# Kernel optimization log

Measured on AMD Instinct MI355X. Metric: run time of the kernel, lower is better.

The kernel has to match this reference:

```python
import jax, jax.numpy as jnp
import numpy as np

ALPHA, GAMMA = 0.25, 2.0
SPARSITY_PENALTY = 1.0
FOCAL_W, SPARSITY_W, CONC_W = 1.0, 0.8, 1.5
CONC_INNER_W = 1.0  # ConcentrationLoss(concentration_weight=1.0)


def setup_inputs() -> dict:
    key = jax.random.key(0)
    k1, k2 = jax.random.split(key)
    B, C, H, W = 16, 20, 256, 256
    pred = jax.random.normal(k1, (B, C, H, W), dtype=jnp.float32)
    target = (jax.random.uniform(k2, (B, C, H, W)) < 0.05).astype(jnp.float32)
    return {"pred": pred, "target": target}


def reference(pred, target):
    B, C, H, W = pred.shape
    p = jax.nn.sigmoid(pred)

    # ---- Focal loss ----
    is_pos = target == 1.0
    pt = jnp.where(is_pos, p, 1.0 - p)
    alpha_t = jnp.where(is_pos, ALPHA, 1.0 - ALPHA)
    focal = jnp.mean(-alpha_t * (1.0 - pt) ** GAMMA * jnp.log(pt + 1e-8))

    # ---- Sparsity loss ----
    sparsity = jnp.mean((pred - target) ** 2) + SPARSITY_PENALTY * jnp.mean(jnp.abs(pred))

    # ---- Concentration loss (vectorized over (b, c)) ----
    y = jnp.arange(H, dtype=jnp.float32)[:, None]   # [H,1]
    x = jnp.arange(W, dtype=jnp.float32)[None, :]   # [1,W]
    mass = target.sum(axis=(2, 3))                  # [B,C]
    valid = mass > 0
    safe_mass = jnp.where(valid, mass, 1.0)
    cy = jnp.einsum('bchw,hw->bc', target, jnp.broadcast_to(y, (H, W))) / safe_mass
    cx = jnp.einsum('bchw,hw->bc', target, jnp.broadcast_to(x, (H, W))) / safe_mass
    # squared distance to per-(b,c) target centroid: [B,C,H,W]
    dsq = (y[None, None] - cy[:, :, None, None]) ** 2 + (x[None, None] - cx[:, :, None, None]) ** 2
    per_sample = jnp.mean(p * dsq, axis=(2, 3))     # [B,C]
    n_valid = valid.sum()
    conc_sum = jnp.sum(jnp.where(valid, per_sample, 0.0))
    concentration = jnp.where(
        n_valid > 0,
        conc_sum / jnp.maximum(n_valid, 1).astype(jnp.float32),
        0.0,
    ) * CONC_INNER_W

    total = FOCAL_W * focal + SPARSITY_W * sparsity + CONC_W * concentration
    return total, focal, sparsity, concentration
```

## Files before the change

kernel.cpp:

```cpp
#include <hip/hip_runtime.h>
#include <math.h>

constexpr int Bn = 16, Cn = 20, Hn = 256, Wn = 256;
constexpr int BCn = Bn * Cn;
constexpr int HWn = Hn * Wn;
constexpr int SPLIT = 8;
constexpr int NBLK = BCn * SPLIT;
constexpr int CHUNK = HWn / SPLIT;
constexpr int TPB = 256;
constexpr int V4 = CHUNK / (TPB * 4);
constexpr int NSLOT = 10;

__device__ inline float wave_reduce(float v) {
    #pragma unroll
    for (int o = 32; o > 0; o >>= 1) v += __shfl_down(v, o, 64);
    return v;
}

__global__ __launch_bounds__(TPB) void partials_kernel(
        const float* __restrict__ pred, const float* __restrict__ target,
        float* __restrict__ ws) {
    const int blk = blockIdx.x;
    const int bc = blk >> 3;
    const int chunk = blk & (SPLIT - 1);
    const long long base = (long long)bc * HWn + (long long)chunk * CHUNK;
    const float4* __restrict__ p4 = (const float4*)(pred + base);
    const float4* __restrict__ t4 = (const float4*)(target + base);
    const int tid = threadIdx.x;

    float acc[NSLOT];
    #pragma unroll
    for (int k = 0; k < NSLOT; k++) acc[k] = 0.f;

    const int e_base = chunk * CHUNK + tid * 4;
    const float x0 = (float)(e_base & 255);
    const float x1 = x0 + 1.f, x2 = x0 + 2.f, x3 = x0 + 3.f;
    const float xs[4]  = {x0, x1, x2, x3};
    const float xxs[4] = {x0 * x0, x1 * x1, x2 * x2, x3 * x3};
    float y = (float)(e_base >> 8);

    float4 pc = p4[tid];
    float4 tc = t4[tid];

    #pragma unroll
    for (int i = 0; i < V4; i++) {
        float4 pn, tn;
        if (i + 1 < V4) {
            pn = p4[(i + 1) * TPB + tid];
            tn = t4[(i + 1) * TPB + tid];
        }
        const float yy = y * y;
        const float pvals[4] = {pc.x, pc.y, pc.z, pc.w};
        const float tvals[4] = {tc.x, tc.y, tc.z, tc.w};
        #pragma unroll
        for (int j = 0; j < 4; j++) {
            const float v = pvals[j];
            const float t = tvals[j];
            const float x = xs[j];
            const float e = __expf(-v);
            const float p = __builtin_amdgcn_rcpf(1.0f + e);
            const bool pos = (t > 0.5f);
            const float lp = __logf(p);
            const float lpt = pos ? lp : lp - v;
            const float om = pos ? 1.0f - p : p;
            const float at = pos ? 0.25f : 0.75f;
            acc[7] = fmaf(at * lpt, om * om, acc[7]);
            const float d = v - t;
            acc[8] = fmaf(d, d, acc[8]);
            acc[9] += fabsf(v);
            acc[0] += t;
            acc[1] = fmaf(t, y, acc[1]);
            acc[2] = fmaf(t, x, acc[2]);
            acc[3] += p;
            acc[4] = fmaf(p, y, acc[4]);
            acc[5] = fmaf(p, x, acc[5]);
            acc[6] = fmaf(p, yy + xxs[j], acc[6]);
        }
        y += 4.0f;
        if (i + 1 < V4) { pc = pn; tc = tn; }
    }

    __shared__ float lds[TPB / 64][NSLOT];
    const int lane = tid & 63, wave = tid >> 6;
    #pragma unroll
    for (int k = 0; k < NSLOT; k++) {
        const float r = wave_reduce(acc[k]);
        if (lane == 0) lds[wave][k] = r;
    }
    __syncthreads();
    if (tid < NSLOT) {
        float s = 0.f;
        #pragma unroll
        for (int w = 0; w < TPB / 64; w++) s += lds[w][tid];
        ws[blk * NSLOT + tid] = s;
    }
}

__global__ __launch_bounds__(512) void finalize_kernel(
        const float* __restrict__ ws, float* __restrict__ out) {
    const int tid = threadIdx.x;

    float conc_sum = 0.f, nvalid = 0.f;
    if (tid < BCn) {
        float mass = 0, sty = 0, stx = 0, sp = 0, spy = 0, spx = 0, sprr = 0;
        for (int s = 0; s < SPLIT; s++) {
            const float* w = ws + (size_t)(tid * SPLIT + s) * NSLOT;
            mass += w[0]; sty += w[1]; stx += w[2]; sp += w[3];
            spy  += w[4]; spx += w[5]; sprr += w[6];
        }
        const bool valid = mass > 0.f;
        const float sm = valid ? mass : 1.0f;
        const float cy = sty / sm, cx = stx / sm;
        const float pdsq = sprr - 2.f * cy * spy - 2.f * cx * spx
                         + (cy * cy + cx * cx) * sp;
        conc_sum = valid ? (pdsq / (float)HWn) : 0.f;
        nvalid   = valid ? 1.f : 0.f;
    }

    float foc = 0.f, sq = 0.f, ab = 0.f;
    for (int blk = tid; blk < NBLK; blk += 512) {
        const float* w = ws + (size_t)blk * NSLOT;
        foc += w[7]; sq += w[8]; ab += w[9];
    }

    __shared__ float lds[8][5];
    const int lane = tid & 63, wave = tid >> 6;
    float vals[5] = {conc_sum, nvalid, foc, sq, ab};
    #pragma unroll
    for (int k = 0; k < 5; k++) {
        const float r = wave_reduce(vals[k]);
        if (lane == 0) lds[wave][k] = r;
    }
    __syncthreads();

    if (tid == 0) {
        float tot[5];
        #pragma unroll
        for (int k = 0; k < 5; k++) {
            float s = 0.f;
            #pragma unroll
            for (int w = 0; w < 8; w++) s += lds[w][k];
            tot[k] = s;
        }
        const float NTOT = (float)Bn * Cn * Hn * Wn;
        const float focal = -tot[2] / NTOT;
        const float sparsity = tot[3] / NTOT + tot[4] / NTOT;
        const float concentration =
            (tot[1] > 0.f) ? (tot[0] / fmaxf(tot[1], 1.f)) : 0.f;
        const float total = 1.0f * focal + 0.8f * sparsity + 1.5f * concentration;
        out[0] = total;
        out[1] = focal;
        out[2] = sparsity;
        out[3] = concentration;
    }
}

extern "C" void kernel_launch(void* const* d_in, const int* in_sizes, int n_in,
                              void* d_out, int out_size, void* d_ws, size_t ws_size,
                              hipStream_t stream) {
    const float* pred   = (const float*)d_in[0];
    const float* target = (const float*)d_in[1];
    float* out = (float*)d_out;
    float* ws  = (float*)d_ws;

    partials_kernel<<<NBLK, TPB, 0, stream>>>(pred, target, ws);
    finalize_kernel<<<1, 512, 0, stream>>>(ws, out);
}
```

Before: 187.9 us.

## Use branchless log2-domain focal math, halve split, transpose workspace layout

Rewrites the per-element focal loss in base-2 (exp2/log2 builtins) with branchless fmaf selects driven by the binary target, and applies the ln2 scale once in the finalize step. Row-constant y terms are hoisted out of the inner 4-element loop by accumulating per-float4 sums of t and p. SPLIT drops from 8 to 4, so each block handles twice as many elements, and launch bounds now request 8 blocks per CU. The workspace is stored slot-major so the 320-thread finalize reads it with coalesced float4 loads. The branchless math relies on targets being exactly 0 or 1, and fewer blocks means less latency hiding.

```diff
diff --git a/kernel.cpp b/kernel.cpp
--- a/kernel.cpp
+++ b/kernel.cpp
@@ -4,7 +4,7 @@
 constexpr int Bn = 16, Cn = 20, Hn = 256, Wn = 256;
 constexpr int BCn = Bn * Cn;
 constexpr int HWn = Hn * Wn;
-constexpr int SPLIT = 8;
+constexpr int SPLIT = 4;
 constexpr int NBLK = BCn * SPLIT;
 constexpr int CHUNK = HWn / SPLIT;
 constexpr int TPB = 256;
@@ -17,11 +17,11 @@
     return v;
 }
 
-__global__ __launch_bounds__(TPB) void partials_kernel(
+__global__ __launch_bounds__(TPB, 8) void partials_kernel(
         const float* __restrict__ pred, const float* __restrict__ target,
         float* __restrict__ ws) {
     const int blk = blockIdx.x;
-    const int bc = blk >> 3;
+    const int bc = blk >> 2;
     const int chunk = blk & (SPLIT - 1);
     const long long base = (long long)bc * HWn + (long long)chunk * CHUNK;
     const float4* __restrict__ p4 = (const float4*)(pred + base);
@@ -34,10 +34,11 @@
 
     const int e_base = chunk * CHUNK + tid * 4;
     const float x0 = (float)(e_base & 255);
-    const float x1 = x0 + 1.f, x2 = x0 + 2.f, x3 = x0 + 3.f;
-    const float xs[4]  = {x0, x1, x2, x3};
-    const float xxs[4] = {x0 * x0, x1 * x1, x2 * x2, x3 * x3};
+    const float xs[4]  = {x0, x0 + 1.f, x0 + 2.f, x0 + 3.f};
+    const float xxs[4] = {xs[0] * xs[0], xs[1] * xs[1], xs[2] * xs[2], xs[3] * xs[3]};
     float y = (float)(e_base >> 8);
+
+    constexpr float L2E = 1.44269504088896f;
 
     float4 pc = p4[tid];
     float4 tc = t4[tid];
@@ -50,32 +51,36 @@
             tn = t4[(i + 1) * TPB + tid];
         }
         const float yy = y * y;
-        const float pvals[4] = {pc.x, pc.y, pc.z, pc.w};
-        const float tvals[4] = {tc.x, tc.y, tc.z, tc.w};
+        const float pv[4] = {pc.x, pc.y, pc.z, pc.w};
+        const float tv[4] = {tc.x, tc.y, tc.z, tc.w};
+        float st4 = 0.f, sp4 = 0.f;
         #pragma unroll
         for (int j = 0; j < 4; j++) {
-            const float v = pvals[j];
-            const float t = tvals[j];
-            const float x = xs[j];
-            const float e = __expf(-v);
-            const float p = __builtin_amdgcn_rcpf(1.0f + e);
-            const bool pos = (t > 0.5f);
-            const float lp = __logf(p);
-            const float lpt = pos ? lp : lp - v;
-            const float om = pos ? 1.0f - p : p;
-            const float at = pos ? 0.25f : 0.75f;
-            acc[7] = fmaf(at * lpt, om * om, acc[7]);
+            const float v = pv[j];
+            const float t = tv[j];
+            const float u  = v * L2E;
+            const float e  = __builtin_amdgcn_exp2f(-u);
+            const float p  = __builtin_amdgcn_rcpf(1.0f + e);
+            const float l2p = __builtin_amdgcn_logf(p);
+            const float l2pt = fmaf(t, u, l2p - u);
+            const float w1 = fmaf(p, -2.0f, 1.0f);
+            const float om = fmaf(t, w1, p);
+            const float at = fmaf(t, -0.5f, 0.75f);
+            acc[7] = fmaf(at * l2pt, om * om, acc[7]);
             const float d = v - t;
             acc[8] = fmaf(d, d, acc[8]);
             acc[9] += fabsf(v);
-            acc[0] += t;
-            acc[1] = fmaf(t, y, acc[1]);
-            acc[2] = fmaf(t, x, acc[2]);
-            acc[3] += p;
-            acc[4] = fmaf(p, y, acc[4]);
-            acc[5] = fmaf(p, x, acc[5]);
-            acc[6] = fmaf(p, yy + xxs[j], acc[6]);
+            st4 += t;
+            acc[2] = fmaf(t, xs[j], acc[2]);
+            sp4 += p;
+            acc[5] = fmaf(p, xs[j], acc[5]);
+            acc[6] = fmaf(p, xxs[j], acc[6]);
         }
+        acc[0] += st4;
+        acc[1] = fmaf(st4, y, acc[1]);
+        acc[3] += sp4;
+        acc[4] = fmaf(sp4, y, acc[4]);
+        acc[6] = fmaf(sp4, yy, acc[6]);
         y += 4.0f;
         if (i + 1 < V4) { pc = pn; tc = tn; }
     }
@@ -92,40 +97,37 @@
         float s = 0.f;
         #pragma unroll
         for (int w = 0; w < TPB / 64; w++) s += lds[w][tid];
-        ws[blk * NSLOT + tid] = s;
+        ws[tid * NBLK + blk] = s;
     }
 }
 
-__global__ __launch_bounds__(512) void finalize_kernel(
+__global__ __launch_bounds__(320) void finalize_kernel(
         const float* __restrict__ ws, float* __restrict__ out) {
     const int tid = threadIdx.x;
+    const float4* __restrict__ w4 = (const float4*)ws;
 
-    float conc_sum = 0.f, nvalid = 0.f;
-    if (tid < BCn) {
-        float mass = 0, sty = 0, stx = 0, sp = 0, spy = 0, spx = 0, sprr = 0;
-        for (int s = 0; s < SPLIT; s++) {
-            const float* w = ws + (size_t)(tid * SPLIT + s) * NSLOT;
-            mass += w[0]; sty += w[1]; stx += w[2]; sp += w[3];
-            spy  += w[4]; spx += w[5]; sprr += w[6];
-        }
-        const bool valid = mass > 0.f;
-        const float sm = valid ? mass : 1.0f;
-        const float cy = sty / sm, cx = stx / sm;
-        const float pdsq = sprr - 2.f * cy * spy - 2.f * cx * spx
-                         + (cy * cy + cx * cx) * sp;
-        conc_sum = valid ? (pdsq / (float)HWn) : 0.f;
-        nvalid   = valid ? 1.f : 0.f;
+    float s[NSLOT];
+    #pragma unroll
+    for (int k = 0; k < NSLOT; k++) {
+        const float4 v = w4[k * (NBLK / 4) + tid];
+        s[k] = v.x + v.y + v.z + v.w;
     }
 
-    float foc = 0.f, sq = 0.f, ab = 0.f;
-    for (int blk = tid; blk < NBLK; blk += 512) {
-        const float* w = ws + (size_t)blk * NSLOT;
-        foc += w[7]; sq += w[8]; ab += w[9];
-    }
+    const float mass = s[0];
+    const bool valid = mass > 0.f;
+    const float sm = valid ? mass : 1.0f;
+    const float cy = s[1] / sm, cx = s[2] / sm;
+    const float pdsq = s[6] - 2.f * cy * s[4] - 2.f * cx * s[5]
+                     + (cy * cy + cx * cx) * s[3];
+    float vals[5];
+    vals[0] = valid ? (pdsq / (float)HWn) : 0.f;
+    vals[1] = valid ? 1.f : 0.f;
+    vals[2] = s[7];
+    vals[3] = s[8];
+    vals[4] = s[9];
 
-    __shared__ float lds[8][5];
+    __shared__ float lds[5][5];
     const int lane = tid & 63, wave = tid >> 6;
-    float vals[5] = {conc_sum, nvalid, foc, sq, ab};
     #pragma unroll
     for (int k = 0; k < 5; k++) {
         const float r = wave_reduce(vals[k]);
@@ -137,13 +139,14 @@
         float tot[5];
         #pragma unroll
         for (int k = 0; k < 5; k++) {
-            float s = 0.f;
+            float acc = 0.f;
             #pragma unroll
-            for (int w = 0; w < 8; w++) s += lds[w][k];
-            tot[k] = s;
+            for (int w = 0; w < 5; w++) acc += lds[w][k];
+            tot[k] = acc;
         }
         const float NTOT = (float)Bn * Cn * Hn * Wn;
-        const float focal = -tot[2] / NTOT;
+        constexpr float LN2 = 0.69314718055994531f;
+        const float focal = -LN2 * tot[2] / NTOT;
         const float sparsity = tot[3] / NTOT + tot[4] / NTOT;
         const float concentration =
             (tot[1] > 0.f) ? (tot[0] / fmaxf(tot[1], 1.f)) : 0.f;
@@ -164,5 +167,5 @@
     float* ws  = (float*)d_ws;
 
     partials_kernel<<<NBLK, TPB, 0, stream>>>(pred, target, ws);
-    finalize_kernel<<<1, 512, 0, stream>>>(ws, out);
+    finalize_kernel<<<1, 320, 0, stream>>>(ws, out);
 }
```

After: 410.1 us. 118% more time.
